# Kernel tuning notes

Measured on AMD Instinct MI355X. Metric: run time of the kernel, lower is better.

## Reference

```python
import jax, jax.numpy as jnp
import numpy as np

HID = 256
IN_DIM = 256
OUT_DIM = 10
L_CYCLES = 6
H_CYCLES = 3
BATCH = 131072
LN_EPS = 1e-5


def _layernorm(v, w, b):
    mu = jnp.mean(v, axis=-1, keepdims=True)
    var = jnp.mean(jnp.square(v - mu), axis=-1, keepdims=True)
    return (v - mu) * jax.lax.rsqrt(var + LN_EPS) * w + b


def setup_inputs() -> dict:
    key = jax.random.key(0)
    ks = jax.random.split(key, 12)
    s = lambda fan_in: 1.0 / np.sqrt(fan_in)
    inp = {
        "x": jax.random.normal(ks[0], (BATCH, IN_DIM), dtype=jnp.float32),
        "W_in": jax.random.uniform(ks[1], (IN_DIM, HID), jnp.float32, -s(IN_DIM), s(IN_DIM)),
        "b_in": jnp.zeros((HID,), jnp.float32),
        "y_init": jax.random.normal(ks[2], (1, HID), dtype=jnp.float32) * 0.02,
        "W_up": jax.random.uniform(ks[3], (HID, 4 * HID), jnp.float32, -s(HID), s(HID)),
        "b_up": jnp.zeros((4 * HID,), jnp.float32),
        "W_down": jax.random.uniform(ks[4], (4 * HID, HID), jnp.float32, -s(4 * HID), s(4 * HID)),
        "b_down": jnp.zeros((HID,), jnp.float32),
        "ln_w": jnp.ones((HID,), jnp.float32),
        "ln_b": jnp.zeros((HID,), jnp.float32),
        "W_comb": jax.random.uniform(ks[5], (2 * HID, HID), jnp.float32, -s(2 * HID), s(2 * HID)),
        "b_comb": jnp.zeros((HID,), jnp.float32),
        "W_yt": jax.random.uniform(ks[6], (HID, HID), jnp.float32, -s(HID), s(HID)),
        "b_yt": jnp.zeros((HID,), jnp.float32),
        "W_head": jax.random.uniform(ks[7], (HID, OUT_DIM), jnp.float32, -s(HID), s(HID)),
        "b_head": jnp.zeros((OUT_DIM,), jnp.float32),
    }
    return inp


def reference(x, W_in, b_in, y_init, W_up, b_up, W_down, b_down, ln_w, ln_b,
              W_comb, b_comb, W_yt, b_yt, W_head, b_head):
    z = x @ W_in + b_in                      # [B, H]
    y = jnp.broadcast_to(y_init, (x.shape[0], HID))
    for _ in range(H_CYCLES):
        for _ in range(L_CYCLES):
            h = jax.nn.gelu(z @ W_up + b_up, approximate=False)
            h = h @ W_down + b_down
            z = _layernorm(z + h, ln_w, ln_b)
        combined = jnp.concatenate([z, y], axis=-1)   # [B, 2H]
        h = jax.nn.gelu(combined @ W_comb + b_comb, approximate=False)
        y = y + h @ W_yt + b_yt
    return y @ W_head + b_head
```

## Files before the change

kernel.cpp:

```cpp
#include <hip/hip_runtime.h>

typedef _Float16 h16;
typedef h16 h16x8 __attribute__((ext_vector_type(8)));
typedef float f32x4 __attribute__((ext_vector_type(4)));

#define MFMA16(a, b, c) __builtin_amdgcn_mfma_f32_16x16x32_f16(a, b, c, 0, 0, 0)

typedef __attribute__((address_space(1))) const char gconst_char;
typedef __attribute__((address_space(3))) char lds_char;
#define GL_LDS16(g, l) __builtin_amdgcn_global_load_lds((gconst_char*)(g), (lds_char*)(l), 16, 0, 0)

#define WIN_OFF   0
#define WIN_CSH   17408
#define WUP_OFF   (WIN_OFF + 8 * WIN_CSH)
#define WUP_CSH   17408
#define WDN_OFF   (WUP_OFF + 32 * WUP_CSH)
#define WDN_CSH   20480
#define WCOMB_OFF (WDN_OFF + 32 * WDN_CSH)
#define WCOMB_CSH 33792
#define WYT_OFF   (WCOMB_OFF + 8 * WCOMB_CSH)
#define WYT_CSH   20480
#define WHEAD_OFF (WYT_OFF + 8 * WYT_CSH)
#define WHEAD_SZ  9216
#define ZY_OFF    (WHEAD_OFF + WHEAD_SZ)
#define ZY_BYTES  (131072UL * 512UL * 2UL)

#define L_WUP0 0
#define L_WUP1 17408
#define L_WDN0 34816
#define L_WDN1 55296
#define L_HS   75776
#define L_BUP  96256
#define L_BDN  100352
#define L_LNW  101376
#define L_LNB  102400
#define SMEM_MEGA 103424

#define C_WC0 0
#define C_WC1 33792
#define C_WY0 67584
#define C_WY1 88064
#define C_GS  108544
#define C_BC  129024
#define C_BY  130048
#define SMEM_COMB 131072

#define SMEM_HEAD 9216

__device__ __forceinline__ void stage_calls(const char* src, char* dst, int calls, int wave,
                                            int nw, int lane) {
  for (int i = wave; i < calls; i += nw)
    GL_LDS16(src + i * 1024 + lane * 16, dst + i * 1024);
}

__device__ __forceinline__ float gelu_f(float x) {
  float t = x * (1.5957691216f + 0.0713548354f * x * x);
  float e = __expf(-t);
  return x * __builtin_amdgcn_rcpf(1.0f + e);
}

__global__ void prepA_kernel(const float* __restrict__ src, h16* __restrict__ dst,
                             int K, int KPp, int CHN, int Nsrc, int CSHh, int tot) {
  for (int d = blockIdx.x * 256 + threadIdx.x; d < tot; d += gridDim.x * 256) {
    int chunk = d / CSHh, r = d % CSHh;
    float v = 0.0f;
    if (r < CHN * KPp) {
      int nl = r / KPp, k = r % KPp;
      int n = chunk * CHN + nl;
      if (k < K && n < Nsrc) v = src[(long)k * Nsrc + n];
    }
    dst[d] = (h16)v;
  }
}
__global__ void prepB_kernel(const float* __restrict__ src, h16* __restrict__ dst,
                             int Kc, int KP2p, int N, int CSHh, int tot) {
  for (int d = blockIdx.x * 256 + threadIdx.x; d < tot; d += gridDim.x * 256) {
    int chunk = d / CSHh, r = d % CSHh;
    float v = 0.0f;
    if (r < N * KP2p) {
      int n = r / KP2p, kp = r % KP2p;
      if (kp < Kc) v = src[(long)(chunk * Kc + kp) * N + n];
    }
    dst[d] = (h16)v;
  }
}

__global__ __launch_bounds__(512) void mega_kernel(
    const float* x, h16* zy,
    const char* __restrict__ winP, const char* __restrict__ wupP, const char* __restrict__ wdnP,
    const float* __restrict__ b_in, const float* __restrict__ b_up,
    const float* __restrict__ b_down, const float* __restrict__ ln_w,
    const float* __restrict__ ln_b, int first) {
  extern __shared__ char smem[];
  const int tid = threadIdx.x, wave = tid >> 6, lane = tid & 63;
  const int q = lane >> 4, c = lane & 15;
  const long m0 = (long)blockIdx.x * 256 + wave * 32;

  float* bupL = (float*)(smem + L_BUP);
  float* bdnL = (float*)(smem + L_BDN);
  float* lnwL = (float*)(smem + L_LNW);
  float* lnbL = (float*)(smem + L_LNB);
  for (int i = tid; i < 1024; i += 512) bupL[i] = b_up[i];
  if (tid < 256) { bdnL[tid] = b_down[tid]; lnwL[tid] = ln_w[tid]; lnbL[tid] = ln_b[tid]; }

  f32x4 acc2[2][16];
  h16x8 az[2][8];
  h16* hsH = (h16*)(smem + L_HS + wave * 2560);
  const f32x4 vzero = {0.0f, 0.0f, 0.0f, 0.0f};

  if (first) {
#pragma unroll
    for (int rt = 0; rt < 2; ++rt)
#pragma unroll
      for (int kk = 0; kk < 8; ++kk) {
        const float* p = x + (m0 + rt * 16 + c) * 256 + kk * 32 + q * 8;
        f32x4 u0 = *(const f32x4*)p;
        f32x4 u1 = *(const f32x4*)(p + 4);
        h16x8 a;
        a[0] = (h16)u0[0]; a[1] = (h16)u0[1]; a[2] = (h16)u0[2]; a[3] = (h16)u0[3];
        a[4] = (h16)u1[0]; a[5] = (h16)u1[1]; a[6] = (h16)u1[2]; a[7] = (h16)u1[3];
        az[rt][kk] = a;
      }
#pragma unroll
    for (int rt = 0; rt < 2; ++rt)
#pragma unroll
      for (int nt = 0; nt < 16; ++nt) acc2[rt][nt] = vzero;

    stage_calls(winP, smem + L_WUP0, 17, wave, 8, lane);
    __syncthreads();
#pragma unroll
    for (int ncI = 0; ncI < 8; ++ncI) {
      if (ncI < 7)
        stage_calls(winP + (ncI + 1) * WIN_CSH, smem + (((ncI + 1) & 1) ? L_WUP1 : L_WUP0),
                    17, wave, 8, lane);
      const char* wb = smem + ((ncI & 1) ? L_WUP1 : L_WUP0);
#pragma unroll
      for (int kk = 0; kk < 8; ++kk)
#pragma unroll
        for (int nt = 0; nt < 2; ++nt) {
          h16x8 b = *(const h16x8*)(wb + ((nt * 16 + c) * 264 + kk * 32 + q * 8) * 2);
#pragma unroll
          for (int rt = 0; rt < 2; ++rt)
            acc2[rt][ncI * 2 + nt] = MFMA16(az[rt][kk], b, acc2[rt][ncI * 2 + nt]);
        }
      __syncthreads();
    }
#pragma unroll
    for (int nt = 0; nt < 16; ++nt) {
      float bi = b_in[nt * 16 + c];
#pragma unroll
      for (int rt = 0; rt < 2; ++rt)
#pragma unroll
        for (int r = 0; r < 4; ++r) acc2[rt][nt][r] += bi;
    }
  } else {
#pragma unroll
    for (int rt = 0; rt < 2; ++rt)
#pragma unroll
      for (int kk = 0; kk < 8; ++kk)
        az[rt][kk] = *(const h16x8*)(zy + (m0 + rt * 16 + c) * 512 + kk * 32 + q * 8);
#pragma unroll
    for (int rt = 0; rt < 2; ++rt)
#pragma unroll
      for (int nt = 0; nt < 16; ++nt)
#pragma unroll
        for (int r = 0; r < 4; ++r)
          acc2[rt][nt][r] = (float)zy[(m0 + rt * 16 + q * 4 + r) * 512 + nt * 16 + c];
  }

  for (int it = 0; it < 6; ++it) {
    if (it > 0 || first) {
      h16* zth = (h16*)(smem + wave * 8448);
#pragma unroll
      for (int rt = 0; rt < 2; ++rt) {
#pragma unroll
        for (int nt = 0; nt < 16; ++nt)
#pragma unroll
          for (int r = 0; r < 4; ++r)
            zth[(q * 4 + r) * 264 + nt * 16 + c] = (h16)acc2[rt][nt][r];
#pragma unroll
        for (int kk = 0; kk < 8; ++kk)
          az[rt][kk] = *(const h16x8*)(zth + c * 264 + kk * 32 + q * 8);
      }
    }
    __syncthreads();
    stage_calls(wupP, smem + L_WUP0, 17, wave, 8, lane);
    stage_calls(wdnP, smem + L_WDN0, 20, wave, 8, lane);
    __syncthreads();

    for (int nc = 0; nc < 32; ++nc) {
      if (nc < 31) {
        int nb = (nc + 1) & 1;
        stage_calls(wupP + (nc + 1) * WUP_CSH, smem + (nb ? L_WUP1 : L_WUP0), 17, wave, 8, lane);
        stage_calls(wdnP + (nc + 1) * WDN_CSH, smem + (nb ? L_WDN1 : L_WDN0), 20, wave, 8, lane);
      }
      const char* wub = smem + ((nc & 1) ? L_WUP1 : L_WUP0);
      const char* wdb = smem + ((nc & 1) ? L_WDN1 : L_WDN0);

      f32x4 acc1[2][2];
      acc1[0][0] = vzero; acc1[0][1] = vzero; acc1[1][0] = vzero; acc1[1][1] = vzero;
#pragma unroll
      for (int kk = 0; kk < 8; ++kk)
#pragma unroll
        for (int nt = 0; nt < 2; ++nt) {
          h16x8 b = *(const h16x8*)(wub + ((nt * 16 + c) * 264 + kk * 32 + q * 8) * 2);
#pragma unroll
          for (int rt = 0; rt < 2; ++rt) acc1[rt][nt] = MFMA16(az[rt][kk], b, acc1[rt][nt]);
        }
#pragma unroll
      for (int rt = 0; rt < 2; ++rt)
#pragma unroll
        for (int nt = 0; nt < 2; ++nt) {
          float bu = bupL[nc * 32 + nt * 16 + c];
#pragma unroll
          for (int r = 0; r < 4; ++r) {
            float g = gelu_f(acc1[rt][nt][r] + bu);
            hsH[(rt * 16 + q * 4 + r) * 40 + nt * 16 + c] = (h16)g;
          }
        }
      h16x8 ah[2];
#pragma unroll
      for (int rt = 0; rt < 2; ++rt)
        ah[rt] = *(const h16x8*)(hsH + (rt * 16 + c) * 40 + q * 8);
#pragma unroll
      for (int nt = 0; nt < 16; ++nt) {
        h16x8 b = *(const h16x8*)(wdb + ((nt * 16 + c) * 40 + q * 8) * 2);
#pragma unroll
        for (int rt = 0; rt < 2; ++rt) acc2[rt][nt] = MFMA16(ah[rt], b, acc2[rt][nt]);
      }
      __syncthreads();
    }

#pragma unroll
    for (int rt = 0; rt < 2; ++rt) {
      float sum[4] = {0, 0, 0, 0}, sq[4] = {0, 0, 0, 0};
#pragma unroll
      for (int nt = 0; nt < 16; ++nt) {
        float bd = bdnL[nt * 16 + c];
#pragma unroll
        for (int r = 0; r < 4; ++r) {
          float v = acc2[rt][nt][r] + bd;
          acc2[rt][nt][r] = v;
          sum[r] += v;
          sq[r] += v * v;
        }
      }
#pragma unroll
      for (int r = 0; r < 4; ++r)
#pragma unroll
        for (int m = 1; m < 16; m <<= 1) {
          sum[r] += __shfl_xor(sum[r], m, 16);
          sq[r] += __shfl_xor(sq[r], m, 16);
        }
      float mu[4], rs[4];
#pragma unroll
      for (int r = 0; r < 4; ++r) {
        mu[r] = sum[r] * (1.0f / 256.0f);
        float var = sq[r] * (1.0f / 256.0f) - mu[r] * mu[r];
        rs[r] = __builtin_amdgcn_rsqf(var + 1e-5f);
      }
#pragma unroll
      for (int nt = 0; nt < 16; ++nt) {
        float w = lnwL[nt * 16 + c], bb = lnbL[nt * 16 + c];
#pragma unroll
        for (int r = 0; r < 4; ++r)
          acc2[rt][nt][r] = (acc2[rt][nt][r] - mu[r]) * rs[r] * w + bb;
      }
    }
  }

#pragma unroll
  for (int rt = 0; rt < 2; ++rt)
#pragma unroll
    for (int nt = 0; nt < 16; ++nt)
#pragma unroll
      for (int r = 0; r < 4; ++r)
        zy[(m0 + rt * 16 + q * 4 + r) * 512 + nt * 16 + c] = (h16)acc2[rt][nt][r];
}

__global__ __launch_bounds__(512) void comb_kernel(
    h16* zy, const char* __restrict__ wcP, const char* __restrict__ wytP,
    const float* __restrict__ b_comb, const float* __restrict__ b_yt,
    const float* __restrict__ y_init, int first) {
  extern __shared__ char smem[];
  const int tid = threadIdx.x, wave = tid >> 6, lane = tid & 63;
  const int q = lane >> 4, c = lane & 15;
  const long m0 = (long)blockIdx.x * 256 + wave * 32;

  float* bcL = (float*)(smem + C_BC);
  float* byL = (float*)(smem + C_BY);
  if (tid < 256) { bcL[tid] = b_comb[tid]; byL[tid] = b_yt[tid]; }

  f32x4 acc2[2][16];
  if (first) {
#pragma unroll
    for (int nt = 0; nt < 16; ++nt) {
      float yv = y_init[nt * 16 + c];
#pragma unroll
      for (int rt = 0; rt < 2; ++rt)
#pragma unroll
        for (int r = 0; r < 4; ++r) acc2[rt][nt][r] = yv;
    }
  } else {
#pragma unroll
    for (int rt = 0; rt < 2; ++rt)
#pragma unroll
      for (int nt = 0; nt < 16; ++nt)
#pragma unroll
        for (int r = 0; r < 4; ++r)
          acc2[rt][nt][r] = (float)zy[(m0 + rt * 16 + q * 4 + r) * 512 + 256 + nt * 16 + c];
  }
  h16* gsH = (h16*)(smem + C_GS + wave * 2560);
  const f32x4 vzero = {0.0f, 0.0f, 0.0f, 0.0f};

  stage_calls(wcP, smem + C_WC0, 33, wave, 8, lane);
  stage_calls(wytP, smem + C_WY0, 20, wave, 8, lane);
  __syncthreads();

  for (int nc = 0; nc < 8; ++nc) {
    if (nc < 7) {
      int nb = (nc + 1) & 1;
      stage_calls(wcP + (nc + 1) * WCOMB_CSH, smem + (nb ? C_WC1 : C_WC0), 33, wave, 8, lane);
      stage_calls(wytP + (nc + 1) * WYT_CSH, smem + (nb ? C_WY1 : C_WY0), 20, wave, 8, lane);
    }
    const char* wcb = smem + ((nc & 1) ? C_WC1 : C_WC0);
    const char* wyb = smem + ((nc & 1) ? C_WY1 : C_WY0);

    f32x4 acc1[2][2];
    acc1[0][0] = vzero; acc1[0][1] = vzero; acc1[1][0] = vzero; acc1[1][1] = vzero;
#pragma unroll
    for (int kk = 0; kk < 16; ++kk) {
      h16x8 a[2];
#pragma unroll
      for (int rt = 0; rt < 2; ++rt)
        a[rt] = *(const h16x8*)(zy + (m0 + rt * 16 + c) * 512 + kk * 32 + q * 8);
#pragma unroll
      for (int nt = 0; nt < 2; ++nt) {
        h16x8 b = *(const h16x8*)(wcb + ((nt * 16 + c) * 520 + kk * 32 + q * 8) * 2);
#pragma unroll
        for (int rt = 0; rt < 2; ++rt) acc1[rt][nt] = MFMA16(a[rt], b, acc1[rt][nt]);
      }
    }
#pragma unroll
    for (int rt = 0; rt < 2; ++rt)
#pragma unroll
      for (int nt = 0; nt < 2; ++nt) {
        float bc = bcL[nc * 32 + nt * 16 + c];
#pragma unroll
        for (int r = 0; r < 4; ++r) {
          float g = gelu_f(acc1[rt][nt][r] + bc);
          gsH[(rt * 16 + q * 4 + r) * 40 + nt * 16 + c] = (h16)g;
        }
      }
    h16x8 ah[2];
#pragma unroll
    for (int rt = 0; rt < 2; ++rt)
      ah[rt] = *(const h16x8*)(gsH + (rt * 16 + c) * 40 + q * 8);
#pragma unroll
    for (int nt = 0; nt < 16; ++nt) {
      h16x8 b = *(const h16x8*)(wyb + ((nt * 16 + c) * 40 + q * 8) * 2);
#pragma unroll
      for (int rt = 0; rt < 2; ++rt) acc2[rt][nt] = MFMA16(ah[rt], b, acc2[rt][nt]);
    }
    __syncthreads();
  }

#pragma unroll
  for (int nt = 0; nt < 16; ++nt) {
    float by = byL[nt * 16 + c];
#pragma unroll
    for (int rt = 0; rt < 2; ++rt)
#pragma unroll
      for (int r = 0; r < 4; ++r)
        zy[(m0 + rt * 16 + q * 4 + r) * 512 + 256 + nt * 16 + c] = (h16)(acc2[rt][nt][r] + by);
  }
}

__global__ __launch_bounds__(256) void head_kernel(const h16* zy, const char* __restrict__ whP,
                                                   const float* __restrict__ b_head,
                                                   float* __restrict__ out) {
  extern __shared__ char smem[];
  const int tid = threadIdx.x, wave = tid >> 6, lane = tid & 63;
  const int q = lane >> 4, c = lane & 15;
  const long m0 = (long)blockIdx.x * 128 + wave * 32;

  stage_calls(whP, smem, 9, wave, 4, lane);
  __syncthreads();

  f32x4 acc[2];
  const f32x4 vzero = {0.0f, 0.0f, 0.0f, 0.0f};
  acc[0] = vzero; acc[1] = vzero;
#pragma unroll
  for (int kk = 0; kk < 8; ++kk) {
    h16x8 b = *(const h16x8*)(smem + (c * 264 + kk * 32 + q * 8) * 2);
#pragma unroll
    for (int rt = 0; rt < 2; ++rt) {
      h16x8 a = *(const h16x8*)(zy + (m0 + rt * 16 + c) * 512 + 256 + kk * 32 + q * 8);
      acc[rt] = MFMA16(a, b, acc[rt]);
    }
  }
  if (c < 10) {
    float bh = b_head[c];
#pragma unroll
    for (int rt = 0; rt < 2; ++rt)
#pragma unroll
      for (int r = 0; r < 4; ++r)
        out[(m0 + rt * 16 + q * 4 + r) * 10 + c] = acc[rt][r] + bh;
  }
}

extern "C" void kernel_launch(void* const* d_in, const int* in_sizes, int n_in, void* d_out,
                              int out_size, void* d_ws, size_t ws_size, hipStream_t stream) {
  (void)in_sizes; (void)n_in; (void)out_size;
  const float* x      = (const float*)d_in[0];
  const float* W_in   = (const float*)d_in[1];
  const float* b_in   = (const float*)d_in[2];
  const float* y_init = (const float*)d_in[3];
  const float* W_up   = (const float*)d_in[4];
  const float* b_up   = (const float*)d_in[5];
  const float* W_down = (const float*)d_in[6];
  const float* b_down = (const float*)d_in[7];
  const float* ln_w   = (const float*)d_in[8];
  const float* ln_b   = (const float*)d_in[9];
  const float* W_comb = (const float*)d_in[10];
  const float* b_comb = (const float*)d_in[11];
  const float* W_yt   = (const float*)d_in[12];
  const float* b_yt   = (const float*)d_in[13];
  const float* W_head = (const float*)d_in[14];
  const float* b_head = (const float*)d_in[15];

  char* ws = (char*)d_ws;
  h16* winP   = (h16*)(ws + WIN_OFF);
  h16* wupP   = (h16*)(ws + WUP_OFF);
  h16* wdnP   = (h16*)(ws + WDN_OFF);
  h16* wcombP = (h16*)(ws + WCOMB_OFF);
  h16* wytP   = (h16*)(ws + WYT_OFF);
  h16* wheadP = (h16*)(ws + WHEAD_OFF);
  h16* zy = (ws_size >= (size_t)ZY_OFF + ZY_BYTES) ? (h16*)(ws + ZY_OFF) : (h16*)d_in[0];

  hipFuncSetAttribute((const void*)mega_kernel, hipFuncAttributeMaxDynamicSharedMemorySize,
                      SMEM_MEGA);
  hipFuncSetAttribute((const void*)comb_kernel, hipFuncAttributeMaxDynamicSharedMemorySize,
                      SMEM_COMB);

  {
    int tot;
    tot = 8 * (WIN_CSH / 2);
    prepA_kernel<<<dim3((tot + 255) / 256), dim3(256), 0, stream>>>(W_in, winP, 256, 264, 32, 256, WIN_CSH / 2, tot);
    tot = 32 * (WUP_CSH / 2);
    prepA_kernel<<<dim3((tot + 255) / 256), dim3(256), 0, stream>>>(W_up, wupP, 256, 264, 32, 1024, WUP_CSH / 2, tot);
    tot = 8 * (WCOMB_CSH / 2);
    prepA_kernel<<<dim3((tot + 255) / 256), dim3(256), 0, stream>>>(W_comb, wcombP, 512, 520, 32, 256, WCOMB_CSH / 2, tot);
    tot = WHEAD_SZ / 2;
    prepA_kernel<<<dim3((tot + 255) / 256), dim3(256), 0, stream>>>(W_head, wheadP, 256, 264, 16, 10, WHEAD_SZ / 2, tot);
    tot = 32 * (WDN_CSH / 2);
    prepB_kernel<<<dim3((tot + 255) / 256), dim3(256), 0, stream>>>(W_down, wdnP, 32, 40, 256, WDN_CSH / 2, tot);
    tot = 8 * (WYT_CSH / 2);
    prepB_kernel<<<dim3((tot + 255) / 256), dim3(256), 0, stream>>>(W_yt, wytP, 32, 40, 256, WYT_CSH / 2, tot);
  }

  for (int h = 0; h < 3; ++h) {
    mega_kernel<<<dim3(512), dim3(512), SMEM_MEGA, stream>>>(
        x, zy, (const char*)winP, (const char*)wupP, (const char*)wdnP, b_in, b_up, b_down,
        ln_w, ln_b, (h == 0) ? 1 : 0);
    comb_kernel<<<dim3(512), dim3(512), SMEM_COMB, stream>>>(
        zy, (const char*)wcombP, (const char*)wytP, b_comb, b_yt, y_init, (h == 0) ? 1 : 0);
  }
  head_kernel<<<dim3(1024), dim3(256), SMEM_HEAD, stream>>>(zy, (const char*)wheadP, b_head,
                                                            (float*)d_out);
}
```

Measured before the change: 4.057 ms.

## Shrink mega kernel blocks, drop padding on down weights, coalesce z/y I/O via LDS

The mega kernel now runs 256-thread blocks of 128 rows over 1024 blocks, which lowers LDS use so more blocks may fit per CU. The W_down and W_yt chunk padding goes from 40 to 32 halfs, shrinking staged bytes, but the unpadded layout risks LDS bank conflicts on the B-fragment reads. Bias and LayerNorm parameters are read straight from global memory instead of being copied into LDS. z/y loads and stores pass through an LDS transpose so global accesses become 16-byte vectors instead of scattered 2-byte ones.

```diff
diff --git a/kernel.cpp b/kernel.cpp
--- a/kernel.cpp
+++ b/kernel.cpp
@@ -15,11 +15,11 @@
 #define WUP_OFF   (WIN_OFF + 8 * WIN_CSH)
 #define WUP_CSH   17408
 #define WDN_OFF   (WUP_OFF + 32 * WUP_CSH)
-#define WDN_CSH   20480
+#define WDN_CSH   16384
 #define WCOMB_OFF (WDN_OFF + 32 * WDN_CSH)
 #define WCOMB_CSH 33792
 #define WYT_OFF   (WCOMB_OFF + 8 * WCOMB_CSH)
-#define WYT_CSH   20480
+#define WYT_CSH   16384
 #define WHEAD_OFF (WYT_OFF + 8 * WYT_CSH)
 #define WHEAD_SZ  9216
 #define ZY_OFF    (WHEAD_OFF + WHEAD_SZ)
@@ -28,22 +28,16 @@
 #define L_WUP0 0
 #define L_WUP1 17408
 #define L_WDN0 34816
-#define L_WDN1 55296
-#define L_HS   75776
-#define L_BUP  96256
-#define L_BDN  100352
-#define L_LNW  101376
-#define L_LNB  102400
-#define SMEM_MEGA 103424
+#define L_WDN1 51200
+#define L_HS   67584
+#define SMEM_MEGA 77824
 
 #define C_WC0 0
 #define C_WC1 33792
 #define C_WY0 67584
-#define C_WY1 88064
-#define C_GS  108544
-#define C_BC  129024
-#define C_BY  130048
-#define SMEM_COMB 131072
+#define C_WY1 83968
+#define C_GS  100352
+#define SMEM_COMB 120832
 
 #define SMEM_HEAD 9216
 
@@ -85,7 +79,7 @@
   }
 }
 
-__global__ __launch_bounds__(512) void mega_kernel(
+__global__ __launch_bounds__(256) void mega_kernel(
     const float* x, h16* zy,
     const char* __restrict__ winP, const char* __restrict__ wupP, const char* __restrict__ wdnP,
     const float* __restrict__ b_in, const float* __restrict__ b_up,
@@ -94,18 +88,12 @@
   extern __shared__ char smem[];
   const int tid = threadIdx.x, wave = tid >> 6, lane = tid & 63;
   const int q = lane >> 4, c = lane & 15;
-  const long m0 = (long)blockIdx.x * 256 + wave * 32;
-
-  float* bupL = (float*)(smem + L_BUP);
-  float* bdnL = (float*)(smem + L_BDN);
-  float* lnwL = (float*)(smem + L_LNW);
-  float* lnbL = (float*)(smem + L_LNB);
-  for (int i = tid; i < 1024; i += 512) bupL[i] = b_up[i];
-  if (tid < 256) { bdnL[tid] = b_down[tid]; lnwL[tid] = ln_w[tid]; lnbL[tid] = ln_b[tid]; }
+  const long m0 = (long)blockIdx.x * 128 + wave * 32;
 
   f32x4 acc2[2][16];
   h16x8 az[2][8];
   h16* hsH = (h16*)(smem + L_HS + wave * 2560);
+  h16* zth = (h16*)(smem) + wave * 4224;
   const f32x4 vzero = {0.0f, 0.0f, 0.0f, 0.0f};
 
   if (first) {
@@ -126,13 +114,13 @@
 #pragma unroll
       for (int nt = 0; nt < 16; ++nt) acc2[rt][nt] = vzero;
 
-    stage_calls(winP, smem + L_WUP0, 17, wave, 8, lane);
+    stage_calls(winP, smem + L_WUP0, 17, wave, 4, lane);
     __syncthreads();
 #pragma unroll
     for (int ncI = 0; ncI < 8; ++ncI) {
       if (ncI < 7)
         stage_calls(winP + (ncI + 1) * WIN_CSH, smem + (((ncI + 1) & 1) ? L_WUP1 : L_WUP0),
-                    17, wave, 8, lane);
+                    17, wave, 4, lane);
       const char* wb = smem + ((ncI & 1) ? L_WUP1 : L_WUP0);
 #pragma unroll
       for (int kk = 0; kk < 8; ++kk)
@@ -155,22 +143,22 @@
     }
   } else {
 #pragma unroll
-    for (int rt = 0; rt < 2; ++rt)
-#pragma unroll
-      for (int kk = 0; kk < 8; ++kk)
+    for (int rt = 0; rt < 2; ++rt) {
+#pragma unroll
+      for (int kk = 0; kk < 8; ++kk) {
         az[rt][kk] = *(const h16x8*)(zy + (m0 + rt * 16 + c) * 512 + kk * 32 + q * 8);
-#pragma unroll
-    for (int rt = 0; rt < 2; ++rt)
+        *(h16x8*)(zth + c * 264 + kk * 32 + q * 8) = az[rt][kk];
+      }
 #pragma unroll
       for (int nt = 0; nt < 16; ++nt)
 #pragma unroll
         for (int r = 0; r < 4; ++r)
-          acc2[rt][nt][r] = (float)zy[(m0 + rt * 16 + q * 4 + r) * 512 + nt * 16 + c];
+          acc2[rt][nt][r] = (float)zth[(q * 4 + r) * 264 + nt * 16 + c];
+    }
   }
 
   for (int it = 0; it < 6; ++it) {
     if (it > 0 || first) {
-      h16* zth = (h16*)(smem + wave * 8448);
 #pragma unroll
       for (int rt = 0; rt < 2; ++rt) {
 #pragma unroll
@@ -184,15 +172,15 @@
       }
     }
     __syncthreads();
-    stage_calls(wupP, smem + L_WUP0, 17, wave, 8, lane);
-    stage_calls(wdnP, smem + L_WDN0, 20, wave, 8, lane);
+    stage_calls(wupP, smem + L_WUP0, 17, wave, 4, lane);
+    stage_calls(wdnP, smem + L_WDN0, 16, wave, 4, lane);
     __syncthreads();
 
     for (int nc = 0; nc < 32; ++nc) {
       if (nc < 31) {
         int nb = (nc + 1) & 1;
-        stage_calls(wupP + (nc + 1) * WUP_CSH, smem + (nb ? L_WUP1 : L_WUP0), 17, wave, 8, lane);
-        stage_calls(wdnP + (nc + 1) * WDN_CSH, smem + (nb ? L_WDN1 : L_WDN0), 20, wave, 8, lane);
+        stage_calls(wupP + (nc + 1) * WUP_CSH, smem + (nb ? L_WUP1 : L_WUP0), 17, wave, 4, lane);
+        stage_calls(wdnP + (nc + 1) * WDN_CSH, smem + (nb ? L_WDN1 : L_WDN0), 16, wave, 4, lane);
       }
       const char* wub = smem + ((nc & 1) ? L_WUP1 : L_WUP0);
       const char* wdb = smem + ((nc & 1) ? L_WDN1 : L_WDN0);
@@ -207,11 +195,13 @@
 #pragma unroll
           for (int rt = 0; rt < 2; ++rt) acc1[rt][nt] = MFMA16(az[rt][kk], b, acc1[rt][nt]);
         }
+      float bu0 = b_up[nc * 32 + c];
+      float bu1 = b_up[nc * 32 + 16 + c];
 #pragma unroll
       for (int rt = 0; rt < 2; ++rt)
 #pragma unroll
         for (int nt = 0; nt < 2; ++nt) {
-          float bu = bupL[nc * 32 + nt * 16 + c];
+          float bu = nt ? bu1 : bu0;
 #pragma unroll
           for (int r = 0; r < 4; ++r) {
             float g = gelu_f(acc1[rt][nt][r] + bu);
@@ -224,7 +214,7 @@
         ah[rt] = *(const h16x8*)(hsH + (rt * 16 + c) * 40 + q * 8);
 #pragma unroll
       for (int nt = 0; nt < 16; ++nt) {
-        h16x8 b = *(const h16x8*)(wdb + ((nt * 16 + c) * 40 + q * 8) * 2);
+        h16x8 b = *(const h16x8*)(wdb + ((nt * 16 + c) * 32 + q * 8) * 2);
 #pragma unroll
         for (int rt = 0; rt < 2; ++rt) acc2[rt][nt] = MFMA16(ah[rt], b, acc2[rt][nt]);
       }
@@ -236,7 +226,7 @@
       float sum[4] = {0, 0, 0, 0}, sq[4] = {0, 0, 0, 0};
 #pragma unroll
       for (int nt = 0; nt < 16; ++nt) {
-        float bd = bdnL[nt * 16 + c];
+        float bd = b_down[nt * 16 + c];
 #pragma unroll
         for (int r = 0; r < 4; ++r) {
           float v = acc2[rt][nt][r] + bd;
@@ -261,7 +251,7 @@
       }
 #pragma unroll
       for (int nt = 0; nt < 16; ++nt) {
-        float w = lnwL[nt * 16 + c], bb = lnbL[nt * 16 + c];
+        float w = ln_w[nt * 16 + c], bb = ln_b[nt * 16 + c];
 #pragma unroll
         for (int r = 0; r < 4; ++r)
           acc2[rt][nt][r] = (acc2[rt][nt][r] - mu[r]) * rs[r] * w + bb;
@@ -270,12 +260,18 @@
   }
 
 #pragma unroll
-  for (int rt = 0; rt < 2; ++rt)
+  for (int rt = 0; rt < 2; ++rt) {
 #pragma unroll
     for (int nt = 0; nt < 16; ++nt)
 #pragma unroll
       for (int r = 0; r < 4; ++r)
-        zy[(m0 + rt * 16 + q * 4 + r) * 512 + nt * 16 + c] = (h16)acc2[rt][nt][r];
+        zth[(q * 4 + r) * 264 + nt * 16 + c] = (h16)acc2[rt][nt][r];
+#pragma unroll
+    for (int kk = 0; kk < 8; ++kk) {
+      h16x8 v = *(const h16x8*)(zth + c * 264 + kk * 32 + q * 8);
+      *(h16x8*)(zy + (m0 + rt * 16 + c) * 512 + kk * 32 + q * 8) = v;
+    }
+  }
 }
 
 __global__ __launch_bounds__(512) void comb_kernel(
@@ -287,9 +283,8 @@
   const int q = lane >> 4, c = lane & 15;
   const long m0 = (long)blockIdx.x * 256 + wave * 32;
 
-  float* bcL = (float*)(smem + C_BC);
-  float* byL = (float*)(smem + C_BY);
-  if (tid < 256) { bcL[tid] = b_comb[tid]; byL[tid] = b_yt[tid]; }
+  h16* gsH = (h16*)(smem + C_GS + wave * 2560);
+  h16* yth = (h16*)(smem) + wave * 4224;
 
   f32x4 acc2[2][16];
   if (first) {
@@ -303,25 +298,31 @@
     }
   } else {
 #pragma unroll
-    for (int rt = 0; rt < 2; ++rt)
+    for (int rt = 0; rt < 2; ++rt) {
+#pragma unroll
+      for (int kk = 0; kk < 8; ++kk) {
+        h16x8 v = *(const h16x8*)(zy + (m0 + rt * 16 + c) * 512 + 256 + kk * 32 + q * 8);
+        *(h16x8*)(yth + c * 264 + kk * 32 + q * 8) = v;
+      }
 #pragma unroll
       for (int nt = 0; nt < 16; ++nt)
 #pragma unroll
         for (int r = 0; r < 4; ++r)
-          acc2[rt][nt][r] = (float)zy[(m0 + rt * 16 + q * 4 + r) * 512 + 256 + nt * 16 + c];
-  }
-  h16* gsH = (h16*)(smem + C_GS + wave * 2560);
+          acc2[rt][nt][r] = (float)yth[(q * 4 + r) * 264 + nt * 16 + c];
+    }
+  }
+  __syncthreads();
   const f32x4 vzero = {0.0f, 0.0f, 0.0f, 0.0f};
 
   stage_calls(wcP, smem + C_WC0, 33, wave, 8, lane);
-  stage_calls(wytP, smem + C_WY0, 20, wave, 8, lane);
+  stage_calls(wytP, smem + C_WY0, 16, wave, 8, lane);
   __syncthreads();
 
   for (int nc = 0; nc < 8; ++nc) {
     if (nc < 7) {
       int nb = (nc + 1) & 1;
       stage_calls(wcP + (nc + 1) * WCOMB_CSH, smem + (nb ? C_WC1 : C_WC0), 33, wave, 8, lane);
-      stage_calls(wytP + (nc + 1) * WYT_CSH, smem + (nb ? C_WY1 : C_WY0), 20, wave, 8, lane);
+      stage_calls(wytP + (nc + 1) * WYT_CSH, smem + (nb ? C_WY1 : C_WY0), 16, wave, 8, lane);
     }
     const char* wcb = smem + ((nc & 1) ? C_WC1 : C_WC0);
     const char* wyb = smem + ((nc & 1) ? C_WY1 : C_WY0);
@@ -341,11 +342,13 @@
         for (int rt = 0; rt < 2; ++rt) acc1[rt][nt] = MFMA16(a[rt], b, acc1[rt][nt]);
       }
     }
+    float bc0 = b_comb[nc * 32 + c];
+    float bc1 = b_comb[nc * 32 + 16 + c];
 #pragma unroll
     for (int rt = 0; rt < 2; ++rt)
 #pragma unroll
       for (int nt = 0; nt < 2; ++nt) {
-        float bc = bcL[nc * 32 + nt * 16 + c];
+        float bc = nt ? bc1 : bc0;
 #pragma unroll
         for (int r = 0; r < 4; ++r) {
           float g = gelu_f(acc1[rt][nt][r] + bc);
@@ -358,7 +361,7 @@
       ah[rt] = *(const h16x8*)(gsH + (rt * 16 + c) * 40 + q * 8);
 #pragma unroll
     for (int nt = 0; nt < 16; ++nt) {
-      h16x8 b = *(const h16x8*)(wyb + ((nt * 16 + c) * 40 + q * 8) * 2);
+      h16x8 b = *(const h16x8*)(wyb + ((nt * 16 + c) * 32 + q * 8) * 2);
 #pragma unroll
       for (int rt = 0; rt < 2; ++rt) acc2[rt][nt] = MFMA16(ah[rt], b, acc2[rt][nt]);
     }
@@ -366,13 +369,19 @@
   }
 
 #pragma unroll
-  for (int nt = 0; nt < 16; ++nt) {
-    float by = byL[nt * 16 + c];
-#pragma unroll
-    for (int rt = 0; rt < 2; ++rt)
+  for (int rt = 0; rt < 2; ++rt) {
+#pragma unroll
+    for (int nt = 0; nt < 16; ++nt) {
+      float by = b_yt[nt * 16 + c];
 #pragma unroll
       for (int r = 0; r < 4; ++r)
-        zy[(m0 + rt * 16 + q * 4 + r) * 512 + 256 + nt * 16 + c] = (h16)(acc2[rt][nt][r] + by);
+        yth[(q * 4 + r) * 264 + nt * 16 + c] = (h16)(acc2[rt][nt][r] + by);
+    }
+#pragma unroll
+    for (int kk = 0; kk < 8; ++kk) {
+      h16x8 v = *(const h16x8*)(yth + c * 264 + kk * 32 + q * 8);
+      *(h16x8*)(zy + (m0 + rt * 16 + c) * 512 + 256 + kk * 32 + q * 8) = v;
+    }
   }
 }
 
@@ -454,13 +463,13 @@
     tot = WHEAD_SZ / 2;
     prepA_kernel<<<dim3((tot + 255) / 256), dim3(256), 0, stream>>>(W_head, wheadP, 256, 264, 16, 10, WHEAD_SZ / 2, tot);
     tot = 32 * (WDN_CSH / 2);
-    prepB_kernel<<<dim3((tot + 255) / 256), dim3(256), 0, stream>>>(W_down, wdnP, 32, 40, 256, WDN_CSH / 2, tot);
+    prepB_kernel<<<dim3((tot + 255) / 256), dim3(256), 0, stream>>>(W_down, wdnP, 32, 32, 256, WDN_CSH / 2, tot);
     tot = 8 * (WYT_CSH / 2);
-    prepB_kernel<<<dim3((tot + 255) / 256), dim3(256), 0, stream>>>(W_yt, wytP, 32, 40, 256, WYT_CSH / 2, tot);
+    prepB_kernel<<<dim3((tot + 255) / 256), dim3(256), 0, stream>>>(W_yt, wytP, 32, 32, 256, WYT_CSH / 2, tot);
   }
 
   for (int h = 0; h < 3; ++h) {
-    mega_kernel<<<dim3(512), dim3(512), SMEM_MEGA, stream>>>(
+    mega_kernel<<<dim3(1024), dim3(256), SMEM_MEGA, stream>>>(
         x, zy, (const char*)winP, (const char*)wupP, (const char*)wdnP, b_in, b_up, b_down,
         ln_w, ln_b, (h == 0) ? 1 : 0);
     comb_kernel<<<dim3(512), dim3(512), SMEM_COMB, stream>>>(
```

Measured after the change: 6.074 ms. +49.7%, slower.
